# Optimization experiments

Hardware: AMD Instinct MI355X
Metric: run time of the kernel (lower is better)

## Reference

```python
import jax, jax.numpy as jnp
import numpy as np

T = 16384       # video length (frames)
C = 7           # out_features = d_model = num surgical phases
F_DIM = 2048    # mstcn_f_dim (spatial feature dim)
LEN_Q = 30      # sliding window length
N_HEADS = 4
D_K = 64        # attn_dim = min(64, mstcn_f_maps=64)
D_FF = 64       # d_ff = mstcn_f_maps


def setup_inputs() -> dict:
    key = jax.random.key(0)
    ks = jax.random.split(key, 10)
    w = lambda i, shape: jax.random.normal(ks[i], shape, jnp.float32) * 0.05
    return {
        "x": jax.random.normal(ks[0], (1, C, T), jnp.float32),
        "long_feature": jax.random.normal(ks[1], (1, T, F_DIM), jnp.float32),
        "W_fc": w(2, (C, F_DIM)),              # nn.Linear(mstcn_f_dim, out_features, bias=False)
        "W_q": w(3, (N_HEADS * D_K, C)),
        "W_k": w(4, (N_HEADS * D_K, C)),
        "W_v": w(5, (N_HEADS * D_K, C)),
        "W_o": w(6, (C, N_HEADS * D_K)),
        "ln1_g": jnp.ones((C,), jnp.float32),
        "ln1_b": jnp.zeros((C,), jnp.float32),
        "W_ff1": w(7, (D_FF, C)),
        "W_ff2": w(8, (C, D_FF)),
        "ln2_g": jnp.ones((C,), jnp.float32),
        "ln2_b": jnp.zeros((C,), jnp.float32),
    }


def layer_norm(x, g, b, eps=1e-5):
    mu = x.mean(-1, keepdims=True)
    var = ((x - mu) ** 2).mean(-1, keepdims=True)
    return (x - mu) * jax.lax.rsqrt(var + eps) * g + b


def reference(x, long_feature, W_fc, W_q, W_k, W_v, W_o, ln1_g, ln1_b, W_ff1, W_ff2, ln2_g, ln2_b):
    # --- vectorized sliding-window (replaces the Python loop of zeros/cat/stack) ---
    feats = x[0].T                                            # (T, C)
    padded = jnp.concatenate([jnp.zeros((LEN_Q - 1, C), feats.dtype), feats], axis=0)
    idx = jnp.arange(T)[:, None] + jnp.arange(LEN_Q)[None, :]  # window ends at frame i
    inputs = padded[idx]                                       # (T, LEN_Q, C)

    # --- spatial embedding: feas = tanh(fc(long_feature)).transpose(0,1) ---
    feas = jnp.tanh(long_feature[0] @ W_fc.T)[:, None, :]      # (T, 1, C)

    # --- decoder layer: cross MHA(query=feas, kv=inputs) + residual + LN ---
    q = (feas @ W_q.T).reshape(T, 1, N_HEADS, D_K).transpose(0, 2, 1, 3)       # (T,H,1,Dk)
    k = (inputs @ W_k.T).reshape(T, LEN_Q, N_HEADS, D_K).transpose(0, 2, 1, 3)  # (T,H,Lq,Dk)
    v = (inputs @ W_v.T).reshape(T, LEN_Q, N_HEADS, D_K).transpose(0, 2, 1, 3)  # (T,H,Lq,Dk)
    scores = jnp.einsum('thqd,thkd->thqk', q, k) / np.float32(np.sqrt(D_K))
    attn = jax.nn.softmax(scores, axis=-1)
    ctx = jnp.einsum('thqk,thkd->thqd', attn, v)
    ctx = ctx.transpose(0, 2, 1, 3).reshape(T, 1, N_HEADS * D_K)
    out = layer_norm(ctx @ W_o.T + feas, ln1_g, ln1_b)         # (T, 1, C)

    # --- position-wise FFN + residual + LN ---
    ff = jax.nn.relu(out @ W_ff1.T) @ W_ff2.T
    out = layer_norm(ff + out, ln2_g, ln2_b)
    return out[:, 0]                                           # (T, C) per-frame logits
```

## Files before the change

kernel.cpp:

```cpp
#include <hip/hip_runtime.h>
#include <math.h>

#define T_FRAMES 16384
#define FDIM 2048
#define LQ 30
#define FR 4
#define BF 64

__global__ __launch_bounds__(448) void setup_kernel(
    const float* __restrict__ Wq, const float* __restrict__ Wk,
    const float* __restrict__ Wv, const float* __restrict__ Wo,
    float* __restrict__ AM) {
  const int e = threadIdx.x;
  if (e >= 392) return;
  const int which = e / 196;
  const int r = e % 196;
  const int h = r / 49;
  const int rr = r % 49;
  const int c = rr / 7;
  const int c2 = rr % 7;
  float s = 0.0f;
  if (which == 0) {
    for (int d = 0; d < 64; ++d)
      s = fmaf(Wq[(h * 64 + d) * 7 + c], Wk[(h * 64 + d) * 7 + c2], s);
  } else {
    for (int d = 0; d < 64; ++d)
      s = fmaf(Wo[c * 256 + h * 64 + d], Wv[(h * 64 + d) * 7 + c2], s);
  }
  AM[e] = s;
}

__global__ __launch_bounds__(256, 4) void feas_kernel(
    const float* __restrict__ lf,
    const float* __restrict__ Wfc,
    float* __restrict__ feas) {
  const int tid = threadIdx.x;
  const int lane = tid & 63;
  const int wave = tid >> 6;
  const int gw = blockIdx.x * 4 + wave;
  const int t0 = gw * FR;
  const float* lfp = lf + (size_t)t0 * FDIM + lane * 4;

  float acc[FR][7];
#pragma unroll
  for (int fr = 0; fr < FR; ++fr)
#pragma unroll
    for (int c = 0; c < 7; ++c) acc[fr][c] = 0.0f;

#pragma unroll
  for (int ch = 0; ch < 8; ++ch) {
    float4 a[FR];
#pragma unroll
    for (int fr = 0; fr < FR; ++fr)
      a[fr] = *(const float4*)(lfp + fr * FDIM + ch * 256);
    float4 w[7];
#pragma unroll
    for (int c = 0; c < 7; ++c)
      w[c] = *(const float4*)(Wfc + c * FDIM + ch * 256 + lane * 4);
#pragma unroll
    for (int fr = 0; fr < FR; ++fr)
#pragma unroll
      for (int c = 0; c < 7; ++c)
        acc[fr][c] = fmaf(a[fr].x, w[c].x, fmaf(a[fr].y, w[c].y,
                     fmaf(a[fr].z, w[c].z, fmaf(a[fr].w, w[c].w, acc[fr][c]))));
  }

#pragma unroll
  for (int fr = 0; fr < FR; ++fr)
#pragma unroll
    for (int c = 0; c < 7; ++c)
#pragma unroll
      for (int off = 1; off < 64; off <<= 1)
        acc[fr][c] += __shfl_xor(acc[fr][c], off, 64);

  float v = acc[0][0];
#pragma unroll
  for (int fr = 0; fr < FR; ++fr)
#pragma unroll
    for (int c = 0; c < 7; ++c)
      if (lane == fr * 7 + c) v = acc[fr][c];
  if (lane < FR * 7) feas[(size_t)t0 * 7 + lane] = tanhf(v);
}

__global__ __launch_bounds__(256) void attn_kernel(
    const float* __restrict__ x,
    const float* __restrict__ feas_g,
    const float* __restrict__ AM,
    const float* __restrict__ W1,
    const float* __restrict__ W2,
    const float* __restrict__ ln1g, const float* __restrict__ ln1b,
    const float* __restrict__ ln2g, const float* __restrict__ ln2b,
    float* __restrict__ out) {
  __shared__ float AM_s[392];
  __shared__ float ft[(BF + LQ - 1) * 7];
  __shared__ float feas_s[BF][7];
  __shared__ float hpart[BF][4][7];

  const int tid = threadIdx.x;
  const int t0 = blockIdx.x * BF;

  for (int i = tid; i < 392; i += 256) AM_s[i] = AM[i];
  for (int i = tid; i < (BF + LQ - 1) * 7; i += 256) {
    const int row = i / 7, c = i % 7;
    const int s = t0 - (LQ - 1) + row;
    ft[i] = (s >= 0) ? x[c * T_FRAMES + s] : 0.0f;
  }
  for (int i = tid; i < BF * 7; i += 256)
    feas_s[i / 7][i % 7] = feas_g[(size_t)t0 * 7 + i];
  __syncthreads();

  {
    const int f = tid >> 2;
    const int h = tid & 3;
    float fe[7];
#pragma unroll
    for (int c = 0; c < 7; ++c) fe[c] = feas_s[f][c];

    const float* Ah = AM_s + h * 49;
    const float* Mh = AM_s + 196 + h * 49;
    float qk[7];
#pragma unroll
    for (int c2 = 0; c2 < 7; ++c2) {
      float s = 0.0f;
#pragma unroll
      for (int c = 0; c < 7; ++c) s = fmaf(fe[c], Ah[c * 7 + c2], s);
      qk[c2] = s * 0.125f;
    }
    const float* frow = &ft[f * 7];
    float sc[LQ];
    float m = -1e30f;
#pragma unroll
    for (int j = 0; j < LQ; ++j) {
      const float* r = frow + j * 7;
      float s = 0.0f;
#pragma unroll
      for (int c2 = 0; c2 < 7; ++c2) s = fmaf(qk[c2], r[c2], s);
      sc[j] = s;
      m = fmaxf(m, s);
    }
    float sum = 0.0f;
    float wsum[7] = {0, 0, 0, 0, 0, 0, 0};
#pragma unroll
    for (int j = 0; j < LQ; ++j) {
      const float p = __expf(sc[j] - m);
      sum += p;
      const float* r = frow + j * 7;
#pragma unroll
      for (int c2 = 0; c2 < 7; ++c2) wsum[c2] = fmaf(p, r[c2], wsum[c2]);
    }
    const float inv = 1.0f / sum;
#pragma unroll
    for (int c = 0; c < 7; ++c) {
      float s = 0.0f;
#pragma unroll
      for (int c2 = 0; c2 < 7; ++c2) s = fmaf(Mh[c * 7 + c2], wsum[c2], s);
      hpart[f][h][c] = s * inv;
    }
  }
  __syncthreads();

  if (tid < BF) {
    const int f = tid;
    float v[7];
#pragma unroll
    for (int c = 0; c < 7; ++c)
      v[c] = feas_s[f][c] + hpart[f][0][c] + hpart[f][1][c] + hpart[f][2][c] + hpart[f][3][c];

    float mu = 0.0f;
#pragma unroll
    for (int c = 0; c < 7; ++c) mu += v[c];
    mu *= (1.0f / 7.0f);
    float var = 0.0f;
#pragma unroll
    for (int c = 0; c < 7; ++c) { const float d = v[c] - mu; var = fmaf(d, d, var); }
    var *= (1.0f / 7.0f);
    float rs = rsqrtf(var + 1e-5f);
    float o1[7];
#pragma unroll
    for (int c = 0; c < 7; ++c) o1[c] = (v[c] - mu) * rs * ln1g[c] + ln1b[c];

    float ff[7] = {0, 0, 0, 0, 0, 0, 0};
    for (int k = 0; k < 64; ++k) {
      float hk = 0.0f;
#pragma unroll
      for (int c = 0; c < 7; ++c) hk = fmaf(W1[k * 7 + c], o1[c], hk);
      hk = fmaxf(hk, 0.0f);
#pragma unroll
      for (int c = 0; c < 7; ++c) ff[c] = fmaf(W2[c * 64 + k], hk, ff[c]);
    }

#pragma unroll
    for (int c = 0; c < 7; ++c) v[c] = ff[c] + o1[c];
    mu = 0.0f;
#pragma unroll
    for (int c = 0; c < 7; ++c) mu += v[c];
    mu *= (1.0f / 7.0f);
    var = 0.0f;
#pragma unroll
    for (int c = 0; c < 7; ++c) { const float d = v[c] - mu; var = fmaf(d, d, var); }
    var *= (1.0f / 7.0f);
    rs = rsqrtf(var + 1e-5f);
    const int t = t0 + f;
#pragma unroll
    for (int c = 0; c < 7; ++c)
      out[(size_t)t * 7 + c] = (v[c] - mu) * rs * ln2g[c] + ln2b[c];
  }
}

extern "C" void kernel_launch(void* const* d_in, const int* in_sizes, int n_in,
                              void* d_out, int out_size, void* d_ws, size_t ws_size,
                              hipStream_t stream) {
  const float* x    = (const float*)d_in[0];
  const float* lf   = (const float*)d_in[1];
  const float* Wfc  = (const float*)d_in[2];
  const float* Wq   = (const float*)d_in[3];
  const float* Wk   = (const float*)d_in[4];
  const float* Wv   = (const float*)d_in[5];
  const float* Wo   = (const float*)d_in[6];
  const float* ln1g = (const float*)d_in[7];
  const float* ln1b = (const float*)d_in[8];
  const float* W1   = (const float*)d_in[9];
  const float* W2   = (const float*)d_in[10];
  const float* ln2g = (const float*)d_in[11];
  const float* ln2b = (const float*)d_in[12];
  float* out = (float*)d_out;

  float* AM = (float*)d_ws;

  setup_kernel<<<1, 448, 0, stream>>>(Wq, Wk, Wv, Wo, AM);
  feas_kernel<<<T_FRAMES / (FR * 4), 256, 0, stream>>>(lf, Wfc, out);
  attn_kernel<<<T_FRAMES / BF, 256, 0, stream>>>(
      x, out, AM, W1, W2, ln1g, ln1b, ln2g, ln2b, out);
}
```

Before: 245.9 us.

## Stage feature rows in LDS and split the reduction across waves in feas kernel

The feas GEMV kernel now loads 8 consecutive frames of long_feature (64 KB) into shared memory with fully coalesced float4 loads. Each of 8 waves owns a 256-column slice and keeps its Wfc slice in registers, and the partial sums are combined across waves through shared memory. This is meant to improve memory-level parallelism and coalescing on the bandwidth-bound 128 MB read. The cost is 64 KB of LDS per block, which limits occupancy, plus an extra block-level sync and cross-wave reduction.

```diff
diff --git a/kernel.cpp b/kernel.cpp
--- a/kernel.cpp
+++ b/kernel.cpp
@@ -4,7 +4,7 @@
 #define T_FRAMES 16384
 #define FDIM 2048
 #define LQ 30
-#define FR 4
+#define F_BLK 8
 #define BF 64
 
 __global__ __launch_bounds__(448) void setup_kernel(
@@ -30,56 +30,67 @@
   AM[e] = s;
 }
 
-__global__ __launch_bounds__(256, 4) void feas_kernel(
+__global__ __launch_bounds__(512, 4) void feas_kernel(
     const float* __restrict__ lf,
     const float* __restrict__ Wfc,
     float* __restrict__ feas) {
+  __shared__ float lfs[F_BLK * FDIM];
+  __shared__ float red[8][56];
+
   const int tid = threadIdx.x;
   const int lane = tid & 63;
   const int wave = tid >> 6;
-  const int gw = blockIdx.x * 4 + wave;
-  const int t0 = gw * FR;
-  const float* lfp = lf + (size_t)t0 * FDIM + lane * 4;
-
-  float acc[FR][7];
-#pragma unroll
-  for (int fr = 0; fr < FR; ++fr)
-#pragma unroll
-    for (int c = 0; c < 7; ++c) acc[fr][c] = 0.0f;
-
-#pragma unroll
-  for (int ch = 0; ch < 8; ++ch) {
-    float4 a[FR];
-#pragma unroll
-    for (int fr = 0; fr < FR; ++fr)
-      a[fr] = *(const float4*)(lfp + fr * FDIM + ch * 256);
-    float4 w[7];
-#pragma unroll
-    for (int c = 0; c < 7; ++c)
-      w[c] = *(const float4*)(Wfc + c * FDIM + ch * 256 + lane * 4);
-#pragma unroll
-    for (int fr = 0; fr < FR; ++fr)
+  const size_t base = (size_t)blockIdx.x * (F_BLK * FDIM);
+
+  const int col = wave * 256 + lane * 4;
+  float4 w[7];
+#pragma unroll
+  for (int c = 0; c < 7; ++c) w[c] = *(const float4*)(Wfc + c * FDIM + col);
+
+  float4 st[8];
+#pragma unroll
+  for (int r = 0; r < 8; ++r)
+    st[r] = *(const float4*)(lf + base + r * 2048 + tid * 4);
+#pragma unroll
+  for (int r = 0; r < 8; ++r)
+    *(float4*)(&lfs[r * 2048 + tid * 4]) = st[r];
+  __syncthreads();
+
+  float acc[F_BLK][7];
+#pragma unroll
+  for (int f = 0; f < F_BLK; ++f) {
+    const float4 a = *(const float4*)(&lfs[f * FDIM + col]);
+#pragma unroll
+    for (int c = 0; c < 7; ++c)
+      acc[f][c] = fmaf(a.x, w[c].x, fmaf(a.y, w[c].y,
+                  fmaf(a.z, w[c].z, a.w * w[c].w)));
+  }
+
+#pragma unroll
+  for (int f = 0; f < F_BLK; ++f)
+#pragma unroll
+    for (int c = 0; c < 7; ++c)
+#pragma unroll
+      for (int off = 1; off < 64; off <<= 1)
+        acc[f][c] += __shfl_xor(acc[f][c], off, 64);
+
+  if (lane < 56) {
+    float v = acc[0][0];
+#pragma unroll
+    for (int f = 0; f < F_BLK; ++f)
 #pragma unroll
       for (int c = 0; c < 7; ++c)
-        acc[fr][c] = fmaf(a[fr].x, w[c].x, fmaf(a[fr].y, w[c].y,
-                     fmaf(a[fr].z, w[c].z, fmaf(a[fr].w, w[c].w, acc[fr][c]))));
-  }
-
-#pragma unroll
-  for (int fr = 0; fr < FR; ++fr)
-#pragma unroll
-    for (int c = 0; c < 7; ++c)
-#pragma unroll
-      for (int off = 1; off < 64; off <<= 1)
-        acc[fr][c] += __shfl_xor(acc[fr][c], off, 64);
-
-  float v = acc[0][0];
-#pragma unroll
-  for (int fr = 0; fr < FR; ++fr)
-#pragma unroll
-    for (int c = 0; c < 7; ++c)
-      if (lane == fr * 7 + c) v = acc[fr][c];
-  if (lane < FR * 7) feas[(size_t)t0 * 7 + lane] = tanhf(v);
+        if (lane == f * 7 + c) v = acc[f][c];
+    red[wave][lane] = v;
+  }
+  __syncthreads();
+
+  if (tid < 56) {
+    float s = 0.0f;
+#pragma unroll
+    for (int wv = 0; wv < 8; ++wv) s += red[wv][tid];
+    feas[(size_t)blockIdx.x * (F_BLK * 7) + tid] = tanhf(s);
+  }
 }
 
 __global__ __launch_bounds__(256) void attn_kernel(
@@ -228,7 +239,7 @@
   float* AM = (float*)d_ws;
 
   setup_kernel<<<1, 448, 0, stream>>>(Wq, Wk, Wv, Wo, AM);
-  feas_kernel<<<T_FRAMES / (FR * 4), 256, 0, stream>>>(lf, Wfc, out);
+  feas_kernel<<<T_FRAMES / F_BLK, 512, 0, stream>>>(lf, Wfc, out);
   attn_kernel<<<T_FRAMES / BF, 256, 0, stream>>>(
       x, out, AM, W1, W2, ln1g, ln1b, ln2g, ln2b, out);
 }
```

After: 260.8 us. 6.1% more time.
